# Kernel optimization log

Hardware: AMD Instinct MI355X
Metric: run time of the kernel (lower is better)

## Reference

```python
import jax, jax.numpy as jnp
import numpy as np

N = 50000    # nodes
E = 600000   # edges
D = 128      # emb_dim
L = 5        # num_layer
VA = 64      # atom feature vocab (per column)
VB = 8       # bond feature vocab (per column)
BN_EPS = 1e-5


def setup_inputs() -> dict:
    key = jax.random.key(0)
    ks = jax.random.split(key, 10)
    x = jax.random.randint(ks[0], (N, 9), 0, VA)
    edge_index = jax.random.randint(ks[1], (2, E), 0, N)
    edge_attr = jax.random.randint(ks[2], (E, 3), 0, VB)
    edge_weight = jax.random.uniform(ks[3], (E,), dtype=jnp.float32)
    s = 0.05
    atom_emb = jax.random.normal(ks[4], (9, VA, D), dtype=jnp.float32) * s
    bond_emb = jax.random.normal(ks[5], (L, 3, VB, D), dtype=jnp.float32) * s
    W1 = jax.random.normal(ks[6], (L, D, 2 * D), dtype=jnp.float32) / np.sqrt(D)
    b1 = jnp.zeros((L, 2 * D), jnp.float32)
    bn1_g = jnp.ones((L, 2 * D), jnp.float32)
    bn1_b = jnp.zeros((L, 2 * D), jnp.float32)
    W2 = jax.random.normal(ks[7], (L, 2 * D, D), dtype=jnp.float32) / np.sqrt(2 * D)
    b2 = jnp.zeros((L, D), jnp.float32)
    eps_p = jnp.zeros((L,), jnp.float32)       # GIN eps per layer
    bn_g = jnp.ones((L, D), jnp.float32)       # outer BatchNorm per layer
    bn_b = jnp.zeros((L, D), jnp.float32)
    return dict(x=x, edge_index=edge_index, edge_attr=edge_attr, edge_weight=edge_weight,
                atom_emb=atom_emb, bond_emb=bond_emb, W1=W1, b1=b1, bn1_g=bn1_g,
                bn1_b=bn1_b, W2=W2, b2=b2, eps_p=eps_p, bn_g=bn_g, bn_b=bn_b)


def _bn(z, g, b):
    # training-mode batch norm over the node dimension
    m = z.mean(axis=0)
    v = z.var(axis=0)
    return (z - m) * jax.lax.rsqrt(v + BN_EPS) * g + b


def reference(x, edge_index, edge_attr, edge_weight, atom_emb, bond_emb,
              W1, b1, bn1_g, bn1_b, W2, b2, eps_p, bn_g, bn_b):
    src, dst = edge_index[0], edge_index[1]
    ew = edge_weight[:, None]                                  # [E,1]
    # AtomEncoder: sum of per-column embedding lookups -> [N,D]
    h = sum(atom_emb[f][x[:, f]] for f in range(9))
    for l in range(L):
        # BondEncoder -> [E,D]
        ea = sum(bond_emb[l, f][edge_attr[:, f]] for f in range(3))
        # message: relu(x_j + edge_emb) * edge_weight, scatter-add to dst
        msg = jax.nn.relu(h[src] + ea) * ew                    # [E,D]
        agg = jax.ops.segment_sum(msg, dst, num_segments=N)    # [N,D]
        z = (1.0 + eps_p[l]) * h + agg
        # GIN MLP: Linear -> BN -> ReLU -> Linear
        z = jax.nn.relu(_bn(z @ W1[l] + b1[l], bn1_g[l], bn1_b[l]))
        z = z @ W2[l] + b2[l]
        # outer BatchNorm, ReLU except last layer (dropout is identity at p=0)
        z = _bn(z, bn_g[l], bn_b[l])
        if l < L - 1:
            z = jax.nn.relu(z)
        h = z
    return h  # JK == 'last'
```

## Files before the change

kernel.cpp:

```cpp
#include <hip/hip_runtime.h>

#define NN 50000
#define EE 600000
#define DD 128
#define DD2 256
#define LL 5
#define BN_EPS 1e-5f

typedef __attribute__((ext_vector_type(8))) _Float16 half8;
typedef __attribute__((ext_vector_type(4))) float f32x4;

__device__ inline unsigned short f2h_bits(float f) {
    _Float16 h = (_Float16)f;
    return __builtin_bit_cast(unsigned short, h);
}
__device__ inline float h2f(unsigned short u) {
    return (float)__builtin_bit_cast(_Float16, u);
}
__device__ inline half8 bnrelu8(half8 v, half8 s, half8 t) {
    half8 r = v * s + t;
#pragma unroll
    for (int k = 0; k < 8; k++) r[k] = (r[k] > (_Float16)0) ? r[k] : (_Float16)0;
    return r;
}


__global__ void hist_kernel(const int* __restrict__ dst, int* __restrict__ counts) {
    int e = blockIdx.x * blockDim.x + threadIdx.x;
    if (e < EE) atomicAdd(&counts[dst[e]], 1);
}

__global__ void scan1_kernel(const int* __restrict__ counts, int* __restrict__ row_ptr,
                             int* __restrict__ blksum) {
    __shared__ int tmp[256];
    int i = blockIdx.x * 256 + threadIdx.x;
    int v = (i < NN) ? counts[i] : 0;
    tmp[threadIdx.x] = v;
    __syncthreads();
    for (int off = 1; off < 256; off <<= 1) {
        int x = 0;
        if (threadIdx.x >= off) x = tmp[threadIdx.x - off];
        __syncthreads();
        if (threadIdx.x >= off) tmp[threadIdx.x] += x;
        __syncthreads();
    }
    if (i < NN) row_ptr[i] = tmp[threadIdx.x] - v;
    if (threadIdx.x == 255) blksum[blockIdx.x] = tmp[255];
}

__global__ void scan2_kernel(int* __restrict__ blksum, int nblocks) {
    __shared__ int tmp[256];
    int v = (threadIdx.x < nblocks) ? blksum[threadIdx.x] : 0;
    tmp[threadIdx.x] = v;
    __syncthreads();
    for (int off = 1; off < 256; off <<= 1) {
        int x = 0;
        if (threadIdx.x >= off) x = tmp[threadIdx.x - off];
        __syncthreads();
        if (threadIdx.x >= off) tmp[threadIdx.x] += x;
        __syncthreads();
    }
    blksum[threadIdx.x] = tmp[threadIdx.x] - v;
}

__global__ void scan3_kernel(int* __restrict__ row_ptr, const int* __restrict__ blksum) {
    int i = blockIdx.x * 256 + threadIdx.x;
    if (i < NN) row_ptr[i] += blksum[blockIdx.x];
    if (i == 0) row_ptr[NN] = EE;
}

__global__ void scatter_kernel(const int* __restrict__ dst, const int* __restrict__ src,
                               const int* __restrict__ edge_attr, const float* __restrict__ ew,
                               const int* __restrict__ row_ptr, int* __restrict__ cursor,
                               uint2* __restrict__ edata) {
    int e = blockIdx.x * blockDim.x + threadIdx.x;
    if (e < EE) {
        int d = dst[e];
        int p = row_ptr[d] + atomicAdd(&cursor[d], 1);
        int cid = edge_attr[3 * e + 0] + 8 * edge_attr[3 * e + 1] + 64 * edge_attr[3 * e + 2];
        uint2 v;
        v.x = (unsigned)src[e];
        v.y = (unsigned)cid | ((unsigned)f2h_bits(ew[e]) << 16);
        edata[p] = v;
    }
}


__global__ void prep_tables_kernel(const float* __restrict__ W1, const float* __restrict__ W2,
                                   const float* __restrict__ bond_emb,
                                   unsigned short* __restrict__ W1t,
                                   unsigned short* __restrict__ W2t,
                                   unsigned short* __restrict__ bsum) {
    const int NW = LL * DD * DD2;
    int idx = blockIdx.x * 256 + threadIdx.x;
    if (idx < NW) {
        int l = idx / (DD * DD2);
        int rem = idx - l * DD * DD2;
        int k = rem / DD2, m = rem - k * DD2;
        W1t[(size_t)l * DD * DD2 + (size_t)m * DD + k] = f2h_bits(W1[idx]);
    } else if (idx < 2 * NW) {
        int j = idx - NW;
        int l = j / (DD * DD2);
        int rem = j - l * DD * DD2;
        int k = rem / DD, m = rem - k * DD;
        W2t[(size_t)l * DD * DD2 + (size_t)m * DD2 + k] = f2h_bits(W2[j]);
    } else if (idx < 2 * NW + LL * 512 * DD) {
        int j = idx - 2 * NW;
        int l = j >> 16;
        int rem = j & 65535;
        int cid = rem >> 7, d = rem & 127;
        int a0 = cid & 7, a1 = (cid >> 3) & 7, a2 = cid >> 6;
        const float* base = bond_emb + (size_t)l * 3 * 8 * DD;
        bsum[j] = f2h_bits(base[a0 * DD + d] + base[(8 + a1) * DD + d] + base[(16 + a2) * DD + d]);
    }
}


__global__ void init_h_kernel(const int* __restrict__ x, const float* __restrict__ atom_emb,
                              unsigned short* __restrict__ h) {
    int n = blockIdx.x * 8 + (threadIdx.x >> 5);
    int lane = threadIdx.x & 31;
    float a0 = 0.f, a1 = 0.f, a2 = 0.f, a3 = 0.f;
#pragma unroll
    for (int f = 0; f < 9; f++) {
        int idx = x[n * 9 + f];
        const float4 v = *(const float4*)(atom_emb + ((size_t)(f * 64 + idx) * DD) + lane * 4);
        a0 += v.x; a1 += v.y; a2 += v.z; a3 += v.w;
    }
    ushort4 o;
    o.x = f2h_bits(a0); o.y = f2h_bits(a1); o.z = f2h_bits(a2); o.w = f2h_bits(a3);
    *(ushort4*)(h + (size_t)n * DD + lane * 4) = o;
}


template <bool FUSE>
__global__ void agg_kernel(const unsigned short* __restrict__ hsrc,
                           const float* __restrict__ stats, const float* __restrict__ g,
                           const float* __restrict__ bb, const int* __restrict__ row_ptr,
                           const uint2* __restrict__ edata,
                           const unsigned short* __restrict__ bsum_l,
                           const float* __restrict__ eps_ptr, unsigned short* __restrict__ Aout) {
    int n = blockIdx.x * 8 + (threadIdx.x >> 5);
    int lane = threadIdx.x & 31;
    int c0 = lane * 4;

    float bs[4] = {1.f, 1.f, 1.f, 1.f}, bt[4] = {0.f, 0.f, 0.f, 0.f};
    if (FUSE) {
        float4 sm = *(const float4*)(stats + c0);
        float4 sq = *(const float4*)(stats + DD + c0);
        float4 gg = *(const float4*)(g + c0);
        float4 bv = *(const float4*)(bb + c0);
        float mv[4] = {sm.x, sm.y, sm.z, sm.w};
        float qv[4] = {sq.x, sq.y, sq.z, sq.w};
        float gv[4] = {gg.x, gg.y, gg.z, gg.w};
        float bbv[4] = {bv.x, bv.y, bv.z, bv.w};
#pragma unroll
        for (int k = 0; k < 4; k++) {
            float mean = mv[k] * (1.f / NN);
            float var = qv[k] * (1.f / NN) - mean * mean;
            bs[k] = gv[k] * rsqrtf(var + BN_EPS);
            bt[k] = bbv[k] - mean * bs[k];
        }
    }

    auto accum = [&](uint2 ed, uint2 hz, uint2 bz, float* acc) {
        float w = h2f((unsigned short)(ed.y >> 16));
        unsigned int hw[2] = {hz.x, hz.y}, bw[2] = {bz.x, bz.y};
#pragma unroll
        for (int k = 0; k < 2; k++) {
            float hv0 = h2f((unsigned short)(hw[k] & 0xffff));
            float hv1 = h2f((unsigned short)(hw[k] >> 16));
            if (FUSE) {
                hv0 = fmaxf(hv0 * bs[2 * k] + bt[2 * k], 0.f);
                hv1 = fmaxf(hv1 * bs[2 * k + 1] + bt[2 * k + 1], 0.f);
            }
            float m0 = fmaxf(hv0 + h2f((unsigned short)(bw[k] & 0xffff)), 0.f);
            float m1 = fmaxf(hv1 + h2f((unsigned short)(bw[k] >> 16)), 0.f);
            acc[2 * k] += m0 * w;
            acc[2 * k + 1] += m1 * w;
        }
    };

    int beg = row_ptr[n], end = row_ptr[n + 1];
    float acc[4] = {0.f, 0.f, 0.f, 0.f};
    int i = beg;
    for (; i + 4 <= end; i += 4) {
        uint2 e0 = edata[i], e1 = edata[i + 1], e2 = edata[i + 2], e3 = edata[i + 3];
        uint2 h0 = *(const uint2*)(hsrc + (size_t)e0.x * DD + c0);
        uint2 b0 = *(const uint2*)(bsum_l + (size_t)(e0.y & 0xffff) * DD + c0);
        uint2 h1 = *(const uint2*)(hsrc + (size_t)e1.x * DD + c0);
        uint2 b1 = *(const uint2*)(bsum_l + (size_t)(e1.y & 0xffff) * DD + c0);
        uint2 h2 = *(const uint2*)(hsrc + (size_t)e2.x * DD + c0);
        uint2 b2 = *(const uint2*)(bsum_l + (size_t)(e2.y & 0xffff) * DD + c0);
        uint2 h3 = *(const uint2*)(hsrc + (size_t)e3.x * DD + c0);
        uint2 b3 = *(const uint2*)(bsum_l + (size_t)(e3.y & 0xffff) * DD + c0);
        accum(e0, h0, b0, acc);
        accum(e1, h1, b1, acc);
        accum(e2, h2, b2, acc);
        accum(e3, h3, b3, acc);
    }
    for (; i < end; i++) {
        uint2 e0 = edata[i];
        uint2 h0 = *(const uint2*)(hsrc + (size_t)e0.x * DD + c0);
        uint2 b0 = *(const uint2*)(bsum_l + (size_t)(e0.y & 0xffff) * DD + c0);
        accum(e0, h0, b0, acc);
    }

    float eps1 = 1.f + eps_ptr[0];
    uint2 hz = *(const uint2*)(hsrc + (size_t)n * DD + c0);
    unsigned int hw[2] = {hz.x, hz.y};
    float self[4];
#pragma unroll
    for (int k = 0; k < 2; k++) {
        float hv0 = h2f((unsigned short)(hw[k] & 0xffff));
        float hv1 = h2f((unsigned short)(hw[k] >> 16));
        if (FUSE) {
            hv0 = fmaxf(hv0 * bs[2 * k] + bt[2 * k], 0.f);
            hv1 = fmaxf(hv1 * bs[2 * k + 1] + bt[2 * k + 1], 0.f);
        }
        self[2 * k] = hv0;
        self[2 * k + 1] = hv1;
    }
    ushort4 o;
    o.x = f2h_bits(eps1 * self[0] + acc[0]);
    o.y = f2h_bits(eps1 * self[1] + acc[1]);
    o.z = f2h_bits(eps1 * self[2] + acc[2]);
    o.w = f2h_bits(eps1 * self[3] + acc[3]);
    *(ushort4*)(Aout + (size_t)n * DD + c0) = o;
}


template <int K, int M, int JW, int GX, bool FUSEA>
__global__ __launch_bounds__(256, 2) void mfma_gemm_persist(
    const unsigned short* __restrict__ A, const unsigned short* __restrict__ Bt,
    const float* __restrict__ bias, const float* __restrict__ astats,
    const float* __restrict__ ag, const float* __restrict__ ab,
    unsigned short* __restrict__ C, float* __restrict__ stats) {
    const int KS = K / 32;
    const int GR = (NN + 63) / 64;
    int wave = threadIdx.x >> 6;
    int lane = threadIdx.x & 63;
    int wr = wave >> 1, wc = wave & 1;
    int col0 = blockIdx.y * (JW * 32) + wc * (JW * 16);
    int lr = lane & 15;
    int q = lane >> 4;

    __shared__ _Float16 s_sh[FUSEA ? K : 1], t_sh[FUSEA ? K : 1];
    half8 sa[FUSEA ? KS : 1], ta[FUSEA ? KS : 1];
    if (FUSEA) {
        for (int c = threadIdx.x; c < K; c += 256) {
            float mean = astats[c] * (1.f / NN);
            float var = astats[K + c] * (1.f / NN) - mean * mean;
            float sc = ag[c] * rsqrtf(var + BN_EPS);
            s_sh[c] = (_Float16)sc;
            t_sh[c] = (_Float16)(ab[c] - mean * sc);
        }
        __syncthreads();
#pragma unroll
        for (int ks = 0; ks < KS; ks++) {
            sa[ks] = *(const half8*)(s_sh + ks * 32 + q * 8);
            ta[ks] = *(const half8*)(t_sh + ks * 32 + q * 8);
        }
    }

    half8 b[JW][KS];
#pragma unroll
    for (int j = 0; j < JW; j++) {
        const unsigned short* bp = Bt + (size_t)(col0 + j * 16 + lr) * K + q * 8;
#pragma unroll
        for (int ks = 0; ks < KS; ks++)
            b[j][ks] = __builtin_bit_cast(half8, *(const int4*)(bp + ks * 32));
    }

    float bi[JW];
#pragma unroll
    for (int j = 0; j < JW; j++) bi[j] = bias[col0 + j * 16 + lr];

    float s_acc[JW], sq_acc[JW];
#pragma unroll
    for (int j = 0; j < JW; j++) { s_acc[j] = 0.f; sq_acc[j] = 0.f; }

    for (int rb = blockIdx.x; rb < GR; rb += GX) {
        int row0 = rb * 64 + wr * 32;
        half8 a[2][KS];
#pragma unroll
        for (int i = 0; i < 2; i++) {
            const unsigned short* ap = A + (size_t)(row0 + i * 16 + lr) * K + q * 8;
#pragma unroll
            for (int ks = 0; ks < KS; ks++) {
                half8 av = __builtin_bit_cast(half8, *(const int4*)(ap + ks * 32));
                if (FUSEA) av = bnrelu8(av, sa[ks], ta[ks]);
                a[i][ks] = av;
            }
        }

        f32x4 acc[2][JW];
#pragma unroll
        for (int i = 0; i < 2; i++)
#pragma unroll
            for (int j = 0; j < JW; j++) acc[i][j] = (f32x4){0.f, 0.f, 0.f, 0.f};

#pragma unroll
        for (int ks = 0; ks < KS; ks++)
#pragma unroll
            for (int i = 0; i < 2; i++)
#pragma unroll
                for (int j = 0; j < JW; j++)
                    acc[i][j] = __builtin_amdgcn_mfma_f32_16x16x32_f16(a[i][ks], b[j][ks], acc[i][j], 0, 0, 0);

#pragma unroll
        for (int j = 0; j < JW; j++) {
            int c = col0 + j * 16 + lr;
#pragma unroll
            for (int i = 0; i < 2; i++) {
#pragma unroll
                for (int r = 0; r < 4; r++) {
                    int row = row0 + i * 16 + q * 4 + r;
                    if (row < NN) {
                        float v = acc[i][j][r] + bi[j];
                        C[(size_t)row * M + c] = f2h_bits(v);
                        s_acc[j] += v;
                        sq_acc[j] += v * v;
                    }
                }
            }
        }
    }

#pragma unroll
    for (int j = 0; j < JW; j++) {
        int c = col0 + j * 16 + lr;
        float s = s_acc[j], sq = sq_acc[j];
        s += __shfl_xor(s, 16);
        s += __shfl_xor(s, 32);
        sq += __shfl_xor(sq, 16);
        sq += __shfl_xor(sq, 32);
        if (q == 0) {
            unsafeAtomicAdd(&stats[c], s);
            unsafeAtomicAdd(&stats[M + c], sq);
        }
    }
}


__global__ void bnapply2_last_kernel(const unsigned short* __restrict__ z,
                                     const float* __restrict__ stats, const float* __restrict__ g,
                                     const float* __restrict__ bb, float* __restrict__ fout) {
    __shared__ float s_sh[DD], t_sh[DD];
    if (threadIdx.x < DD) {
        int c = threadIdx.x;
        float mean = stats[c] * (1.f / NN);
        float var = stats[DD + c] * (1.f / NN) - mean * mean;
        float sc = g[c] * rsqrtf(var + BN_EPS);
        s_sh[c] = sc;
        t_sh[c] = bb[c] - mean * sc;
    }
    __syncthreads();
    int i = (blockIdx.x * 256 + threadIdx.x) * 4;
    int c = i & 127;
    uint2 in = *(const uint2*)(z + i);
    float4 out;
    out.x = h2f((unsigned short)(in.x & 0xffff)) * s_sh[c] + t_sh[c];
    out.y = h2f((unsigned short)(in.x >> 16)) * s_sh[c + 1] + t_sh[c + 1];
    out.z = h2f((unsigned short)(in.y & 0xffff)) * s_sh[c + 2] + t_sh[c + 2];
    out.w = h2f((unsigned short)(in.y >> 16)) * s_sh[c + 3] + t_sh[c + 3];
    *(float4*)(fout + i) = out;
}


extern "C" void kernel_launch(void* const* d_in, const int* in_sizes, int n_in,
                              void* d_out, int out_size, void* d_ws, size_t ws_size,
                              hipStream_t stream) {
    const int* x = (const int*)d_in[0];
    const int* edge_index = (const int*)d_in[1];
    const int* edge_attr = (const int*)d_in[2];
    const float* edge_weight = (const float*)d_in[3];
    const float* atom_emb = (const float*)d_in[4];
    const float* bond_emb = (const float*)d_in[5];
    const float* W1 = (const float*)d_in[6];
    const float* b1 = (const float*)d_in[7];
    const float* bn1_g = (const float*)d_in[8];
    const float* bn1_b = (const float*)d_in[9];
    const float* W2 = (const float*)d_in[10];
    const float* b2 = (const float*)d_in[11];
    const float* eps_p = (const float*)d_in[12];
    const float* bn_g = (const float*)d_in[13];
    const float* bn_b = (const float*)d_in[14];
    const int* srcv = edge_index;
    const int* dstv = edge_index + EE;

    char* p = (char*)d_ws;
    auto alloc = [&](size_t bytes) {
        void* r = (void*)p;
        p += (bytes + 255) & ~(size_t)255;
        return r;
    };
    unsigned short* h = (unsigned short*)alloc((size_t)NN * DD * 2);
    unsigned short* A1h = (unsigned short*)alloc((size_t)NN * DD * 2);
    unsigned short* z1 = (unsigned short*)alloc((size_t)NN * DD2 * 2);
    unsigned short* z2 = (unsigned short*)alloc((size_t)NN * DD * 2);
    uint2* edata = (uint2*)alloc((size_t)EE * 8);
    int* counts = (int*)alloc((size_t)NN * 4);
    int* row_ptr = (int*)alloc((size_t)(NN + 1) * 4);
    int* blksum = (int*)alloc(256 * 4);
    unsigned short* W1t = (unsigned short*)alloc((size_t)LL * DD * DD2 * 2);
    unsigned short* W2t = (unsigned short*)alloc((size_t)LL * DD * DD2 * 2);
    unsigned short* bsum = (unsigned short*)alloc((size_t)LL * 512 * DD * 2);
    float* statsAll = (float*)alloc((size_t)(LL * 512 + LL * 256) * 4);
    float* stats1Base = statsAll;
    float* stats2Base = statsAll + LL * 512;

    hipMemsetAsync(counts, 0, (size_t)NN * 4, stream);
    hipMemsetAsync(statsAll, 0, (size_t)(LL * 512 + LL * 256) * 4, stream);
    hist_kernel<<<(EE + 255) / 256, 256, 0, stream>>>(dstv, counts);
    int nblk = (NN + 255) / 256;
    scan1_kernel<<<nblk, 256, 0, stream>>>(counts, row_ptr, blksum);
    scan2_kernel<<<1, 256, 0, stream>>>(blksum, nblk);
    scan3_kernel<<<nblk, 256, 0, stream>>>(row_ptr, blksum);
    hipMemsetAsync(counts, 0, (size_t)NN * 4, stream);
    scatter_kernel<<<(EE + 255) / 256, 256, 0, stream>>>(dstv, srcv, edge_attr, edge_weight,
                                                         row_ptr, counts, edata);
    prep_tables_kernel<<<(2 * LL * DD * DD2 + LL * 512 * DD + 255) / 256, 256, 0, stream>>>(
        W1, W2, bond_emb, W1t, W2t, bsum);
    init_h_kernel<<<NN / 8, 256, 0, stream>>>(x, atom_emb, h);

    for (int l = 0; l < LL; l++) {
        float* stats1 = stats1Base + l * 512;
        float* stats2 = stats2Base + l * 256;
        const unsigned short* bsum_l = bsum + (size_t)l * 512 * DD;

        if (l == 0) {
            agg_kernel<false><<<NN / 8, 256, 0, stream>>>(h, nullptr, nullptr, nullptr, row_ptr,
                                                          edata, bsum_l, eps_p + l, A1h);
        } else {
            agg_kernel<true><<<NN / 8, 256, 0, stream>>>(
                z2, stats2Base + (l - 1) * 256, bn_g + (l - 1) * DD, bn_b + (l - 1) * DD, row_ptr,
                edata, bsum_l, eps_p + l, A1h);
        }

        mfma_gemm_persist<DD, DD2, 4, 256, false><<<dim3(256, 2), 256, 0, stream>>>(
            A1h, W1t + (size_t)l * DD * DD2, b1 + l * DD2, nullptr, nullptr, nullptr, z1, stats1);

        mfma_gemm_persist<DD2, DD, 2, 256, true><<<dim3(256, 2), 256, 0, stream>>>(
            z1, W2t + (size_t)l * DD * DD2, b2 + l * DD, stats1, bn1_g + l * DD2, bn1_b + l * DD2,
            z2, stats2);
    }

    bnapply2_last_kernel<<<NN * DD / 1024, 256, 0, stream>>>(
        z2, stats2Base + (LL - 1) * 256, bn_g + (LL - 1) * DD, bn_b + (LL - 1) * DD,
        (float*)d_out);
}
```

Measured before the change: 693.8 us.

## Fuse both GIN MLP GEMMs into one persistent kernel with grid barrier

Replaces the two per-layer GEMM launches with one persistent kernel of 512 blocks. Each block computes up to two 64-row tiles of the first linear layer and keeps the fp16 intermediate in LDS (swizzled, 64KB) instead of writing z1 to global memory. A software grid barrier then waits for the BN statistics of that layer, and the second GEMM applies BN+ReLU to the LDS data. This removes the z1 global round trip and one launch per layer. In exchange it needs all 512 blocks to be resident at once (risk of deadlock), and the large LDS use lowers occupancy.

Result: slower. 1.221 ms (+76.0%).

```diff
diff --git a/kernel.cpp b/kernel.cpp
--- a/kernel.cpp
+++ b/kernel.cpp
@@ -6,6 +6,8 @@
 #define DD2 256
 #define LL 5
 #define BN_EPS 1e-5f
+#define GXF 512
+#define NT1 782
 
 typedef __attribute__((ext_vector_type(8))) _Float16 half8;
 typedef __attribute__((ext_vector_type(4))) float f32x4;
@@ -22,6 +24,23 @@
 #pragma unroll
     for (int k = 0; k < 8; k++) r[k] = (r[k] > (_Float16)0) ? r[k] : (_Float16)0;
     return r;
+}
+
+__device__ inline void grid_barrier(int* bar) {
+    __syncthreads();
+    if (threadIdx.x == 0) {
+        __threadfence();
+        int t = __hip_atomic_fetch_add(&bar[0], 1, __ATOMIC_ACQ_REL, __HIP_MEMORY_SCOPE_AGENT);
+        if (t == GXF - 1) {
+            __hip_atomic_store(&bar[1], 1, __ATOMIC_RELEASE, __HIP_MEMORY_SCOPE_AGENT);
+        } else {
+            while (__hip_atomic_load(&bar[1], __ATOMIC_ACQUIRE, __HIP_MEMORY_SCOPE_AGENT) == 0) {
+                __builtin_amdgcn_s_sleep(16);
+            }
+        }
+        __threadfence();
+    }
+    __syncthreads();
 }
 
 
@@ -230,114 +249,198 @@
 }
 
 
-template <int K, int M, int JW, int GX, bool FUSEA>
-__global__ __launch_bounds__(256, 2) void mfma_gemm_persist(
-    const unsigned short* __restrict__ A, const unsigned short* __restrict__ Bt,
-    const float* __restrict__ bias, const float* __restrict__ astats,
-    const float* __restrict__ ag, const float* __restrict__ ab,
-    unsigned short* __restrict__ C, float* __restrict__ stats) {
-    const int KS = K / 32;
-    const int GR = (NN + 63) / 64;
-    int wave = threadIdx.x >> 6;
-    int lane = threadIdx.x & 63;
-    int wr = wave >> 1, wc = wave & 1;
-    int col0 = blockIdx.y * (JW * 32) + wc * (JW * 16);
-    int lr = lane & 15;
-    int q = lane >> 4;
-
-    __shared__ _Float16 s_sh[FUSEA ? K : 1], t_sh[FUSEA ? K : 1];
-    half8 sa[FUSEA ? KS : 1], ta[FUSEA ? KS : 1];
-    if (FUSEA) {
-        for (int c = threadIdx.x; c < K; c += 256) {
-            float mean = astats[c] * (1.f / NN);
-            float var = astats[K + c] * (1.f / NN) - mean * mean;
-            float sc = ag[c] * rsqrtf(var + BN_EPS);
-            s_sh[c] = (_Float16)sc;
-            t_sh[c] = (_Float16)(ab[c] - mean * sc);
-        }
-        __syncthreads();
-#pragma unroll
-        for (int ks = 0; ks < KS; ks++) {
-            sa[ks] = *(const half8*)(s_sh + ks * 32 + q * 8);
-            ta[ks] = *(const half8*)(t_sh + ks * 32 + q * 8);
-        }
-    }
-
-    half8 b[JW][KS];
-#pragma unroll
-    for (int j = 0; j < JW; j++) {
-        const unsigned short* bp = Bt + (size_t)(col0 + j * 16 + lr) * K + q * 8;
-#pragma unroll
-        for (int ks = 0; ks < KS; ks++)
-            b[j][ks] = __builtin_bit_cast(half8, *(const int4*)(bp + ks * 32));
-    }
-
-    float bi[JW];
-#pragma unroll
-    for (int j = 0; j < JW; j++) bi[j] = bias[col0 + j * 16 + lr];
-
-    float s_acc[JW], sq_acc[JW];
-#pragma unroll
-    for (int j = 0; j < JW; j++) { s_acc[j] = 0.f; sq_acc[j] = 0.f; }
-
-    for (int rb = blockIdx.x; rb < GR; rb += GX) {
-        int row0 = rb * 64 + wr * 32;
-        half8 a[2][KS];
-#pragma unroll
-        for (int i = 0; i < 2; i++) {
-            const unsigned short* ap = A + (size_t)(row0 + i * 16 + lr) * K + q * 8;
-#pragma unroll
-            for (int ks = 0; ks < KS; ks++) {
-                half8 av = __builtin_bit_cast(half8, *(const int4*)(ap + ks * 32));
-                if (FUSEA) av = bnrelu8(av, sa[ks], ta[ks]);
-                a[i][ks] = av;
-            }
-        }
-
-        f32x4 acc[2][JW];
-#pragma unroll
-        for (int i = 0; i < 2; i++)
-#pragma unroll
-            for (int j = 0; j < JW; j++) acc[i][j] = (f32x4){0.f, 0.f, 0.f, 0.f};
-
-#pragma unroll
-        for (int ks = 0; ks < KS; ks++)
-#pragma unroll
-            for (int i = 0; i < 2; i++)
-#pragma unroll
-                for (int j = 0; j < JW; j++)
-                    acc[i][j] = __builtin_amdgcn_mfma_f32_16x16x32_f16(a[i][ks], b[j][ks], acc[i][j], 0, 0, 0);
-
-#pragma unroll
-        for (int j = 0; j < JW; j++) {
-            int c = col0 + j * 16 + lr;
-#pragma unroll
-            for (int i = 0; i < 2; i++) {
-#pragma unroll
-                for (int r = 0; r < 4; r++) {
-                    int row = row0 + i * 16 + q * 4 + r;
-                    if (row < NN) {
-                        float v = acc[i][j][r] + bi[j];
-                        C[(size_t)row * M + c] = f2h_bits(v);
-                        s_acc[j] += v;
-                        sq_acc[j] += v * v;
+__global__ __launch_bounds__(256, 2) void fused_mlp_kernel(
+    const unsigned short* __restrict__ A, const unsigned short* __restrict__ W1,
+    const float* __restrict__ b1, const unsigned short* __restrict__ W2,
+    const float* __restrict__ b2, const float* __restrict__ g1,
+    const float* __restrict__ bb1, unsigned short* __restrict__ z2,
+    float* __restrict__ stats1, float* __restrict__ stats2, int* bar) {
+    __shared__ __align__(16) char ldsb[65536];
+    const int lane = threadIdx.x & 63;
+    const int wave = threadIdx.x >> 6;
+    const int lr = lane & 15;
+    const int q = lane >> 4;
+    const int swz = (lr & 7) << 4;
+
+    {
+        const int wcol = wave * 64;
+        half8 wf[4][4];
+#pragma unroll
+        for (int jm = 0; jm < 4; jm++) {
+            const unsigned short* p = W1 + (size_t)(wcol + jm * 16 + lr) * DD + q * 8;
+#pragma unroll
+            for (int ks = 0; ks < 4; ks++)
+                wf[jm][ks] = __builtin_bit_cast(half8, *(const int4*)(p + ks * 32));
+        }
+        float bi[4][4];
+#pragma unroll
+        for (int jm = 0; jm < 4; jm++)
+#pragma unroll
+            for (int r = 0; r < 4; r++) bi[jm][r] = b1[wcol + jm * 16 + q * 4 + r];
+
+        float s1[16], sq1[16];
+#pragma unroll
+        for (int k = 0; k < 16; k++) { s1[k] = 0.f; sq1[k] = 0.f; }
+
+        for (int s = 0; s < 2; s++) {
+            int t = blockIdx.x + s * GXF;
+            if (t >= NT1) break;
+            int row0 = t * 64;
+            const unsigned short* ap0 = A + (size_t)(row0 + lr) * DD + q * 8;
+            f32x4 acc[4][4];
+#pragma unroll
+            for (int jm = 0; jm < 4; jm++)
+#pragma unroll
+                for (int in = 0; in < 4; in++) acc[jm][in] = (f32x4){0.f, 0.f, 0.f, 0.f};
+#pragma unroll
+            for (int ks = 0; ks < 4; ks++) {
+                half8 rf[4];
+#pragma unroll
+                for (int in = 0; in < 4; in++)
+                    rf[in] = __builtin_bit_cast(
+                        half8, *(const int4*)(ap0 + (size_t)(in * 16) * DD + ks * 32));
+#pragma unroll
+                for (int jm = 0; jm < 4; jm++)
+#pragma unroll
+                    for (int in = 0; in < 4; in++)
+                        acc[jm][in] = __builtin_amdgcn_mfma_f32_16x16x32_f16(
+                            wf[jm][ks], rf[in], acc[jm][in], 0, 0, 0);
+            }
+            char* slot = ldsb + s * 32768;
+#pragma unroll
+            for (int in = 0; in < 4; in++) {
+                int row = in * 16 + lr;
+                bool rv = (row0 + row) < NN;
+                int rbase = row * 512 + wave * 128;
+#pragma unroll
+                for (int jm = 0; jm < 4; jm++) {
+                    ushort4 o;
+#pragma unroll
+                    for (int r = 0; r < 4; r++) {
+                        float v = acc[jm][in][r] + bi[jm][r];
+                        ((unsigned short*)&o)[r] = f2h_bits(v);
+                        if (rv) {
+                            s1[jm * 4 + r] += v;
+                            sq1[jm * 4 + r] += v * v;
+                        }
+                    }
+                    *(ushort4*)(slot + ((rbase + jm * 32 + q * 8) ^ swz)) = o;
+                }
+            }
+        }
+#pragma unroll
+        for (int k = 0; k < 16; k++) {
+            float a = s1[k], b = sq1[k];
+#pragma unroll
+            for (int m = 1; m < 16; m <<= 1) {
+                a += __shfl_xor(a, m);
+                b += __shfl_xor(b, m);
+            }
+            if (lr == 0) {
+                int c = wcol + (k >> 2) * 16 + q * 4 + (k & 3);
+                unsafeAtomicAdd(&stats1[c], a);
+                unsafeAtomicAdd(&stats1[DD2 + c], b);
+            }
+        }
+    }
+
+    grid_barrier(bar);
+
+    {
+        const int cb2 = wave * 32;
+        half8 sa[8], ta[8];
+#pragma unroll
+        for (int ks = 0; ks < 8; ks++) {
+#pragma unroll
+            for (int e = 0; e < 8; e++) {
+                int c = ks * 32 + q * 8 + e;
+                float sv = __hip_atomic_load(&stats1[c], __ATOMIC_RELAXED,
+                                             __HIP_MEMORY_SCOPE_AGENT);
+                float qv = __hip_atomic_load(&stats1[DD2 + c], __ATOMIC_RELAXED,
+                                             __HIP_MEMORY_SCOPE_AGENT);
+                float mean = sv * (1.f / NN);
+                float var = qv * (1.f / NN) - mean * mean;
+                float sc = g1[c] * rsqrtf(var + BN_EPS);
+                sa[ks][e] = (_Float16)sc;
+                ta[ks][e] = (_Float16)(bb1[c] - mean * sc);
+            }
+        }
+        half8 wf2[2][8];
+#pragma unroll
+        for (int jm = 0; jm < 2; jm++) {
+            const unsigned short* p = W2 + (size_t)(cb2 + jm * 16 + lr) * DD2 + q * 8;
+#pragma unroll
+            for (int ks = 0; ks < 8; ks++)
+                wf2[jm][ks] = __builtin_bit_cast(half8, *(const int4*)(p + ks * 32));
+        }
+        float bi2[2][4];
+#pragma unroll
+        for (int jm = 0; jm < 2; jm++)
+#pragma unroll
+            for (int r = 0; r < 4; r++) bi2[jm][r] = b2[cb2 + jm * 16 + q * 4 + r];
+
+        float s2[8], sq2[8];
+#pragma unroll
+        for (int k = 0; k < 8; k++) { s2[k] = 0.f; sq2[k] = 0.f; }
+
+        for (int s = 0; s < 2; s++) {
+            int t = blockIdx.x + s * GXF;
+            if (t >= NT1) break;
+            int row0 = t * 64;
+            char* slot = ldsb + s * 32768;
+            f32x4 acc[2][4];
+#pragma unroll
+            for (int jm = 0; jm < 2; jm++)
+#pragma unroll
+                for (int in = 0; in < 4; in++) acc[jm][in] = (f32x4){0.f, 0.f, 0.f, 0.f};
+#pragma unroll
+            for (int ks = 0; ks < 8; ks++) {
+                half8 rf[4];
+#pragma unroll
+                for (int in = 0; in < 4; in++) {
+                    int row = in * 16 + lr;
+                    half8 z = *(const half8*)(slot + ((row * 512 + ks * 64 + q * 16) ^ swz));
+                    rf[in] = bnrelu8(z, sa[ks], ta[ks]);
+                }
+#pragma unroll
+                for (int jm = 0; jm < 2; jm++)
+#pragma unroll
+                    for (int in = 0; in < 4; in++)
+                        acc[jm][in] = __builtin_amdgcn_mfma_f32_16x16x32_f16(
+                            wf2[jm][ks], rf[in], acc[jm][in], 0, 0, 0);
+            }
+#pragma unroll
+            for (int in = 0; in < 4; in++) {
+                int row = row0 + in * 16 + lr;
+                if (row < NN) {
+#pragma unroll
+                    for (int jm = 0; jm < 2; jm++) {
+                        ushort4 o;
+#pragma unroll
+                        for (int r = 0; r < 4; r++) {
+                            float v = acc[jm][in][r] + bi2[jm][r];
+                            ((unsigned short*)&o)[r] = f2h_bits(v);
+                            s2[jm * 4 + r] += v;
+                            sq2[jm * 4 + r] += v * v;
+                        }
+                        *(ushort4*)(z2 + (size_t)row * DD + cb2 + jm * 16 + q * 4) = o;
                     }
                 }
             }
         }
-    }
-
-#pragma unroll
-    for (int j = 0; j < JW; j++) {
-        int c = col0 + j * 16 + lr;
-        float s = s_acc[j], sq = sq_acc[j];
-        s += __shfl_xor(s, 16);
-        s += __shfl_xor(s, 32);
-        sq += __shfl_xor(sq, 16);
-        sq += __shfl_xor(sq, 32);
-        if (q == 0) {
-            unsafeAtomicAdd(&stats[c], s);
-            unsafeAtomicAdd(&stats[M + c], sq);
+#pragma unroll
+        for (int k = 0; k < 8; k++) {
+            float a = s2[k], b = sq2[k];
+#pragma unroll
+            for (int m = 1; m < 16; m <<= 1) {
+                a += __shfl_xor(a, m);
+                b += __shfl_xor(b, m);
+            }
+            if (lr == 0) {
+                int c = cb2 + (k >> 2) * 16 + q * 4 + (k & 3);
+                unsafeAtomicAdd(&stats2[c], a);
+                unsafeAtomicAdd(&stats2[DD + c], b);
+            }
         }
     }
 }
@@ -396,8 +499,7 @@
         return r;
     };
     unsigned short* h = (unsigned short*)alloc((size_t)NN * DD * 2);
-    unsigned short* A1h = (unsigned short*)alloc((size_t)NN * DD * 2);
-    unsigned short* z1 = (unsigned short*)alloc((size_t)NN * DD2 * 2);
+    unsigned short* A1h = (unsigned short*)alloc((size_t)(NT1 * 64) * DD * 2);
     unsigned short* z2 = (unsigned short*)alloc((size_t)NN * DD * 2);
     uint2* edata = (uint2*)alloc((size_t)EE * 8);
     int* counts = (int*)alloc((size_t)NN * 4);
@@ -406,12 +508,13 @@
     unsigned short* W1t = (unsigned short*)alloc((size_t)LL * DD * DD2 * 2);
     unsigned short* W2t = (unsigned short*)alloc((size_t)LL * DD * DD2 * 2);
     unsigned short* bsum = (unsigned short*)alloc((size_t)LL * 512 * DD * 2);
-    float* statsAll = (float*)alloc((size_t)(LL * 512 + LL * 256) * 4);
+    float* statsAll = (float*)alloc((size_t)(LL * 512 + LL * 256 + LL * 2) * 4);
     float* stats1Base = statsAll;
     float* stats2Base = statsAll + LL * 512;
+    int* barriers = (int*)(statsAll + LL * 512 + LL * 256);
 
     hipMemsetAsync(counts, 0, (size_t)NN * 4, stream);
-    hipMemsetAsync(statsAll, 0, (size_t)(LL * 512 + LL * 256) * 4, stream);
+    hipMemsetAsync(statsAll, 0, (size_t)(LL * 512 + LL * 256 + LL * 2) * 4, stream);
     hist_kernel<<<(EE + 255) / 256, 256, 0, stream>>>(dstv, counts);
     int nblk = (NN + 255) / 256;
     scan1_kernel<<<nblk, 256, 0, stream>>>(counts, row_ptr, blksum);
@@ -438,12 +541,9 @@
                 edata, bsum_l, eps_p + l, A1h);
         }
 
-        mfma_gemm_persist<DD, DD2, 4, 256, false><<<dim3(256, 2), 256, 0, stream>>>(
-            A1h, W1t + (size_t)l * DD * DD2, b1 + l * DD2, nullptr, nullptr, nullptr, z1, stats1);
-
-        mfma_gemm_persist<DD2, DD, 2, 256, true><<<dim3(256, 2), 256, 0, stream>>>(
-            z1, W2t + (size_t)l * DD * DD2, b2 + l * DD, stats1, bn1_g + l * DD2, bn1_b + l * DD2,
-            z2, stats2);
+        fused_mlp_kernel<<<GXF, 256, 0, stream>>>(
+            A1h, W1t + (size_t)l * DD * DD2, b1 + l * DD2, W2t + (size_t)l * DD * DD2,
+            b2 + l * DD, bn1_g + l * DD2, bn1_b + l * DD2, z2, stats1, stats2, barriers + l * 2);
     }
 
     bnapply2_last_kernel<<<NN * DD / 1024, 256, 0, stream>>>(
```
